# Kernel optimization log

Hardware: AMD Instinct MI355X
Metric: run time of the kernel (lower is better)

## Reference

```python
import jax, jax.numpy as jnp
import numpy as np

N = 50000      # nodes
E = 800000     # edges (before self loops)
F_IN = 128     # num_features
D = 128        # d_graph_layer
L = 3          # n_graph_layer (extra GAT layers after conv1)
DFC = 128      # d_FC_layer
NFC = 2        # n_FC_layer
C = 2          # num_classes
G = 1000       # number of graphs
NEG_SLOPE = 0.2


def setup_inputs() -> dict:
    key = jax.random.key(0)
    ks = jax.random.split(key, 24)
    s = lambda d: 1.0 / np.sqrt(d)
    inp = {
        "x": jax.random.normal(ks[0], (N, F_IN), jnp.float32),
        "energy": jax.random.normal(ks[1], (G, 1), jnp.float32),
        # conv1 params
        "W1": jax.random.normal(ks[2], (F_IN, D), jnp.float32) * s(F_IN),
        "as1": jax.random.normal(ks[3], (D,), jnp.float32) * s(D),
        "ad1": jax.random.normal(ks[4], (D,), jnp.float32) * s(D),
        "b1": jnp.zeros((D,), jnp.float32),
        # stacked convs params
        "Ws": jax.random.normal(ks[5], (L, D, D), jnp.float32) * s(D),
        "ass": jax.random.normal(ks[6], (L, D), jnp.float32) * s(D),
        "ads": jax.random.normal(ks[7], (L, D), jnp.float32) * s(D),
        "bs": jnp.zeros((L, D), jnp.float32),
        # FC head
        "lin0_W": jax.random.normal(ks[8], (D, DFC), jnp.float32) * s(D),
        "lin0_b": jnp.zeros((DFC,), jnp.float32),
        "lin1_W": jax.random.normal(ks[9], (DFC + 1, DFC), jnp.float32) * s(DFC + 1),
        "lin1_b": jnp.zeros((DFC,), jnp.float32),
        "lins_W": jax.random.normal(ks[10], (NFC - 1, DFC, DFC), jnp.float32) * s(DFC),
        "lins_b": jnp.zeros((NFC - 1, DFC), jnp.float32),
        "lin3_W": jax.random.normal(ks[11], (DFC, C), jnp.float32) * s(DFC),
        "lin3_b": jnp.zeros((C,), jnp.float32),
        # graph structure
        "edge_index": jax.random.randint(ks[12], (2, E), 0, N, dtype=jnp.int64),
        "batchs": jnp.sort(jax.random.randint(ks[13], (N,), 0, G, dtype=jnp.int64)),
    }
    return inp


def gat_layer(x, W, a_src, a_dst, b, src, dst):
    # GATConv (heads=1): h = xW; e_ij = LeakyReLU(a_src.h_src + a_dst.h_dst);
    # alpha = softmax over edges grouped by dst; out_i = sum alpha * h_src + b
    h = x @ W                                        # [N, D]
    e = jax.nn.leaky_relu((h @ a_src)[src] + (h @ a_dst)[dst], NEG_SLOPE)  # [E']
    m = jax.ops.segment_max(e, dst, num_segments=N)  # every node has a self loop
    w = jnp.exp(e - m[dst])
    denom = jax.ops.segment_sum(w, dst, num_segments=N)
    alpha = w / denom[dst]
    out = jax.ops.segment_sum(h[src] * alpha[:, None], dst, num_segments=N)
    return out + b


def reference(x, energy, W1, as1, ad1, b1, Ws, ass, ads, bs,
              lin0_W, lin0_b, lin1_W, lin1_b, lins_W, lins_b,
              lin3_W, lin3_b, edge_index, batchs):
    loop = jnp.arange(N, dtype=edge_index.dtype)     # GATConv add_self_loops
    src = jnp.concatenate([edge_index[0], loop])
    dst = jnp.concatenate([edge_index[1], loop])

    h = jax.nn.relu(gat_layer(x, W1, as1, ad1, b1, src, dst))
    for i in range(L):
        h = jax.nn.relu(gat_layer(h, Ws[i], ass[i], ads[i], bs[i], src, dst))

    g = jax.ops.segment_sum(h, batchs, num_segments=G)   # global_add_pool [G, D]
    y = jax.nn.relu(g @ lin0_W + lin0_b)                 # lins[0]
    z = jax.nn.relu(jnp.concatenate([y, energy], axis=1) @ lin1_W + lin1_b)
    z = z + y                                            # residual
    for i in range(NFC - 1):
        z = jax.nn.relu(z @ lins_W[i] + lins_b[i])
    logits = z @ lin3_W + lin3_b
    return jax.nn.log_softmax(logits, axis=1)            # last == 'log'
```

## Files before the change

### kernel.cpp

```cpp
#include <hip/hip_runtime.h>
#include <math.h>

#define NN 50000
#define EE 800000
#define ET 850000
#define DD 128
#define GG 1000
#define SLOPE 0.2f

#define KB   2048
#define NBA  416
#define BSZ  4096
#define NBUK 208

typedef unsigned int  u32;
typedef unsigned short u16;

__device__ __forceinline__ u16 f2h(float f){
  return __builtin_bit_cast(unsigned short, (_Float16)f);
}
__device__ __forceinline__ float hlo(u32 d){
  return (float)__builtin_bit_cast(_Float16, (unsigned short)(d & 0xFFFFu));
}
__device__ __forceinline__ float hhi(u32 d){
  return (float)__builtin_bit_cast(_Float16, (unsigned short)(d >> 16));
}

__global__ void init_k(const int* __restrict__ batchs, int* __restrict__ cnt,
                       int* __restrict__ gstart, int* __restrict__ bcur){
  int n = blockIdx.x*256 + threadIdx.x;
  if (n < NBUK) bcur[n] = 0;
  if (n < NN){
    cnt[n] = 0;
    int b = batchs[n];
    int prev = n ? batchs[n-1] : -1;
    for (int g = prev+1; g <= b; ++g) gstart[g] = n;
    if (n == NN-1){
      for (int g = b+1; g <= GG; ++g) gstart[g] = NN;
    }
  }
}

__global__ void count_k(const int* __restrict__ ei, int* __restrict__ cnt,
                        int* __restrict__ rank){
  int e = blockIdx.x*256 + threadIdx.x;
  if (e < ET){
    int d = (e < EE) ? ei[EE + e] : (e - EE);
    rank[e] = atomicAdd(&cnt[d], 1);
  }
}

__global__ __launch_bounds__(256) void blocksum_k(const int* __restrict__ cnt,
                                                  int* __restrict__ bsum){
  int i = blockIdx.x*256 + threadIdx.x;
  int v = (i < NN) ? cnt[i] : 0;
  #pragma unroll
  for (int o=32;o;o>>=1) v += __shfl_xor(v,o);
  __shared__ int ws[4];
  if ((threadIdx.x & 63) == 0) ws[threadIdx.x>>6] = v;
  __syncthreads();
  if (threadIdx.x == 0) bsum[blockIdx.x] = ws[0]+ws[1]+ws[2]+ws[3];
}

__global__ __launch_bounds__(256) void scanb_k(int* __restrict__ bsum, int nb){
  int tid = threadIdx.x;
  int v = (tid < nb) ? bsum[tid] : 0;
  int lane = tid & 63, wv = tid >> 6;
  int s = v;
  #pragma unroll
  for (int o=1;o<64;o<<=1){ int t = __shfl_up(s,o); if (lane>=o) s += t; }
  __shared__ int ws[4];
  if (lane == 63) ws[wv] = s;
  __syncthreads();
  int woff = 0;
  for (int k=0;k<wv;++k) woff += ws[k];
  if (tid < nb) bsum[tid] = s - v + woff;
}

__global__ __launch_bounds__(256) void scatter_k(const int* __restrict__ cnt,
                                                 const int* __restrict__ bsum,
                                                 int* __restrict__ row_start){
  int i = blockIdx.x*256 + threadIdx.x;
  int v = (i < NN) ? cnt[i] : 0;
  int lane = threadIdx.x & 63, wv = threadIdx.x >> 6;
  int s = v;
  #pragma unroll
  for (int o=1;o<64;o<<=1){ int t = __shfl_up(s,o); if (lane>=o) s += t; }
  __shared__ int ws[4];
  if (lane == 63) ws[wv] = s;
  __syncthreads();
  int woff = 0;
  for (int k=0;k<wv;++k) woff += ws[k];
  int off = s - v + woff + bsum[blockIdx.x];
  if (i < NN) row_start[i] = off;
  if (i == 0) row_start[NN] = ET;
}

__global__ __launch_bounds__(256) void partA_k(const int* __restrict__ ei,
                                               const int* __restrict__ rank,
                                               const int* __restrict__ row_start,
                                               int* __restrict__ bcur,
                                               uint2* __restrict__ stage){
  __shared__ uint2 lpairs[KB];
  __shared__ int lcnt[256], lstart[256], lrun[256], gbase[256];
  __shared__ int ws[4];
  int tid = threadIdx.x;
  int base = blockIdx.x * KB;
  int nE = min(KB, ET - base);
  lcnt[tid] = 0;
  __syncthreads();
  u32 pos_r[KB/256]; u32 src_r[KB/256];
  #pragma unroll
  for (int i=0;i<KB/256;++i){
    int e = base + i*256 + tid;
    u32 p = 0xFFFFFFFFu, s = 0;
    if (e < ET){
      int d, sr;
      if (e < EE){ sr = ei[e]; d = ei[EE + e]; }
      else       { sr = e - EE; d = sr; }
      p = (u32)(row_start[d] + rank[e]);
      s = (u32)sr;
      atomicAdd(&lcnt[p >> 12], 1);
    }
    pos_r[i] = p; src_r[i] = s;
  }
  __syncthreads();
  int v = lcnt[tid];
  int lane = tid & 63, wv = tid >> 6;
  int s = v;
  #pragma unroll
  for (int o=1;o<64;o<<=1){ int t = __shfl_up(s,o); if (lane>=o) s += t; }
  if (lane == 63) ws[wv] = s;
  __syncthreads();
  int woff = 0;
  for (int k=0;k<wv;++k) woff += ws[k];
  int excl = s - v + woff;
  lstart[tid] = excl;
  lrun[tid]   = excl;
  gbase[tid]  = (tid < NBUK && v > 0) ? atomicAdd(&bcur[tid], v) : 0;
  __syncthreads();
  #pragma unroll
  for (int i=0;i<KB/256;++i){
    if (pos_r[i] != 0xFFFFFFFFu){
      int b = pos_r[i] >> 12;
      int slot = atomicAdd(&lrun[b], 1);
      lpairs[slot] = make_uint2(pos_r[i], src_r[i]);
    }
  }
  __syncthreads();
  for (int j = tid; j < nE; j += 256){
    uint2 pr = lpairs[j];
    int b = pr.x >> 12;
    int dest = (b << 12) + gbase[b] + (j - lstart[b]);
    stage[dest] = pr;
  }
}

__global__ __launch_bounds__(256) void partB_k(const uint2* __restrict__ stage,
                                               int* __restrict__ srcs){
  __shared__ int buf[BSZ];
  int b = blockIdx.x, tid = threadIdx.x;
  int base = b << 12;
  int n_b = min(BSZ, ET - base);
  for (int j = tid; j < n_b; j += 256){
    uint2 pr = stage[base + j];
    buf[pr.x - base] = (int)pr.y;
  }
  __syncthreads();
  for (int j = tid; j*4 < n_b; j += 256){
    *(int4*)(srcs + base + j*4) = *(const int4*)(buf + j*4);
  }
}

__global__ __launch_bounds__(256) void gemm128_f_k(const float* __restrict__ A,
                                                   const float* __restrict__ W,
                                                   const float* __restrict__ as,
                                                   const float* __restrict__ ad,
                                                   float* __restrict__ C,
                                                   float* __restrict__ hs,
                                                   float* __restrict__ hd){
  __shared__ float Alt[DD*64];
  __shared__ float Wl[DD*64];
  int tid = threadIdx.x;
  int rbase = blockIdx.x*64;
  for (int it=0; it<8; ++it){
    int i = it*256 + tid;
    int r = i & 63;
    int c4 = i >> 6;
    float4 v = {0.f,0.f,0.f,0.f};
    if (rbase + r < NN) v = *(const float4*)(A + (size_t)(rbase+r)*DD + c4*4);
    Alt[(c4*4+0)*64 + r] = v.x;
    Alt[(c4*4+1)*64 + r] = v.y;
    Alt[(c4*4+2)*64 + r] = v.z;
    Alt[(c4*4+3)*64 + r] = v.w;
  }
  int ry = tid >> 4, cx = tid & 15;
  float hsum[4] = {0.f,0.f,0.f,0.f};
  float hdsum[4] = {0.f,0.f,0.f,0.f};
  for (int jt=0; jt<2; ++jt){
    __syncthreads();
    for (int it=0; it<8; ++it){
      int i = it*256 + tid;
      int k = i >> 4, c4 = i & 15;
      *(float4*)(Wl + k*64 + c4*4) = *(const float4*)(W + k*DD + jt*64 + c4*4);
    }
    __syncthreads();
    float acc[4][4] = {};
    #pragma unroll 8
    for (int k=0;k<DD;++k){
      float4 av = *(const float4*)(Alt + k*64 + ry*4);
      float4 wv = *(const float4*)(Wl + k*64 + cx*4);
      float a[4] = {av.x, av.y, av.z, av.w};
      float b[4] = {wv.x, wv.y, wv.z, wv.w};
      #pragma unroll
      for (int ii=0;ii<4;++ii)
        #pragma unroll
        for (int jj=0;jj<4;++jj)
          acc[ii][jj] += a[ii]*b[jj];
    }
    float4 a_s = *(const float4*)(as + jt*64 + cx*4);
    float4 a_d = *(const float4*)(ad + jt*64 + cx*4);
    #pragma unroll
    for (int ii=0;ii<4;++ii){
      float ds = acc[ii][0]*a_s.x + acc[ii][1]*a_s.y + acc[ii][2]*a_s.z + acc[ii][3]*a_s.w;
      float dd = acc[ii][0]*a_d.x + acc[ii][1]*a_d.y + acc[ii][2]*a_d.z + acc[ii][3]*a_d.w;
      #pragma unroll
      for (int o=1;o<16;o<<=1){ ds += __shfl_xor(ds,o); dd += __shfl_xor(dd,o); }
      hsum[ii] += ds; hdsum[ii] += dd;
    }
    #pragma unroll
    for (int ii=0;ii<4;++ii){
      int r = rbase + ry*4 + ii;
      if (r < NN){
        float4 o = {acc[ii][0], acc[ii][1], acc[ii][2], acc[ii][3]};
        *(float4*)(C + (size_t)r*DD + jt*64 + cx*4) = o;
      }
    }
  }
  if (cx == 0){
    #pragma unroll
    for (int ii=0;ii<4;++ii){
      int r = rbase + ry*4 + ii;
      if (r < NN){ hs[r] = hsum[ii]; hd[r] = hdsum[ii]; }
    }
  }
}

__global__ __launch_bounds__(256) void gemm128_h_k(const float* __restrict__ A,
                                                   const float* __restrict__ W,
                                                   const float* __restrict__ as,
                                                   const float* __restrict__ ad,
                                                   u16* __restrict__ Ch,
                                                   float* __restrict__ hs,
                                                   float* __restrict__ hd){
  __shared__ float Alt[DD*64];
  __shared__ float Wl[DD*64];
  int tid = threadIdx.x;
  int rbase = blockIdx.x*64;
  for (int it=0; it<8; ++it){
    int i = it*256 + tid;
    int r = i & 63;
    int c4 = i >> 6;
    float4 v = {0.f,0.f,0.f,0.f};
    if (rbase + r < NN) v = *(const float4*)(A + (size_t)(rbase+r)*DD + c4*4);
    Alt[(c4*4+0)*64 + r] = v.x;
    Alt[(c4*4+1)*64 + r] = v.y;
    Alt[(c4*4+2)*64 + r] = v.z;
    Alt[(c4*4+3)*64 + r] = v.w;
  }
  int ry = tid >> 4, cx = tid & 15;
  float hsum[4] = {0.f,0.f,0.f,0.f};
  float hdsum[4] = {0.f,0.f,0.f,0.f};
  for (int jt=0; jt<2; ++jt){
    __syncthreads();
    for (int it=0; it<8; ++it){
      int i = it*256 + tid;
      int k = i >> 4, c4 = i & 15;
      *(float4*)(Wl + k*64 + c4*4) = *(const float4*)(W + k*DD + jt*64 + c4*4);
    }
    __syncthreads();
    float acc[4][4] = {};
    #pragma unroll 8
    for (int k=0;k<DD;++k){
      float4 av = *(const float4*)(Alt + k*64 + ry*4);
      float4 wv = *(const float4*)(Wl + k*64 + cx*4);
      float a[4] = {av.x, av.y, av.z, av.w};
      float b[4] = {wv.x, wv.y, wv.z, wv.w};
      #pragma unroll
      for (int ii=0;ii<4;++ii)
        #pragma unroll
        for (int jj=0;jj<4;++jj)
          acc[ii][jj] += a[ii]*b[jj];
    }
    float4 a_s = *(const float4*)(as + jt*64 + cx*4);
    float4 a_d = *(const float4*)(ad + jt*64 + cx*4);
    #pragma unroll
    for (int ii=0;ii<4;++ii){
      float ds = acc[ii][0]*a_s.x + acc[ii][1]*a_s.y + acc[ii][2]*a_s.z + acc[ii][3]*a_s.w;
      float dd = acc[ii][0]*a_d.x + acc[ii][1]*a_d.y + acc[ii][2]*a_d.z + acc[ii][3]*a_d.w;
      #pragma unroll
      for (int o=1;o<16;o<<=1){ ds += __shfl_xor(ds,o); dd += __shfl_xor(dd,o); }
      hsum[ii] += ds; hdsum[ii] += dd;
    }
    #pragma unroll
    for (int ii=0;ii<4;++ii){
      int r = rbase + ry*4 + ii;
      if (r < NN){
        ushort4 o;
        o.x = f2h(acc[ii][0]); o.y = f2h(acc[ii][1]);
        o.z = f2h(acc[ii][2]); o.w = f2h(acc[ii][3]);
        *(ushort4*)(Ch + (size_t)r*DD + jt*64 + cx*4) = o;
      }
    }
  }
  if (cx == 0){
    #pragma unroll
    for (int ii=0;ii<4;++ii){
      int r = rbase + ry*4 + ii;
      if (r < NN){ hs[r] = hsum[ii]; hd[r] = hdsum[ii]; }
    }
  }
}

__global__ __launch_bounds__(256) void gat_agg_f_k(const float* __restrict__ h,
                                                   const float* __restrict__ hs,
                                                   const float* __restrict__ hd,
                                                   const int* __restrict__ row_start,
                                                   const int* __restrict__ srcs,
                                                   const float* __restrict__ bias,
                                                   float* __restrict__ out){
  int node = blockIdx.x*4 + (threadIdx.x >> 6);
  int lane = threadIdx.x & 63;
  if (node >= NN) return;
  int half = lane >> 5;
  int hl   = lane & 31;
  int beg = row_start[node], end = row_start[node+1];
  float hdn = hd[node];
  float m = -INFINITY, denom = 0.f;
  float4 acc = {0.f,0.f,0.f,0.f};
  for (int c=beg; c<end; c+=64){
    int nc = min(64, end-c);
    float e = -INFINITY; int src = 0;
    if (lane < nc){
      src = srcs[c+lane];
      float t = hs[src] + hdn;
      e = (t >= 0.f) ? t : SLOPE*t;
    }
    float cm = e;
    #pragma unroll
    for (int o=32;o;o>>=1) cm = fmaxf(cm, __shfl_xor(cm,o));
    float nm = fmaxf(m, cm);
    float w = (lane < nc) ? expf(e - nm) : 0.f;
    float cs = w;
    #pragma unroll
    for (int o=32;o;o>>=1) cs += __shfl_xor(cs,o);
    float scale = expf(m - nm);
    denom = denom*scale + cs;
    acc.x *= scale; acc.y *= scale; acc.z *= scale; acc.w *= scale;
    m = nm;
    int nh = (nc + 1 - half) >> 1;
    for (int i=0;i<nh;++i){
      int j = 2*i + half;
      float wi = __shfl(w, j);
      int   si = __shfl(src, j);
      float4 hv = *(const float4*)(h + (size_t)si*DD + hl*4);
      acc.x += wi*hv.x; acc.y += wi*hv.y; acc.z += wi*hv.z; acc.w += wi*hv.w;
    }
  }
  acc.x += __shfl_xor(acc.x, 32);
  acc.y += __shfl_xor(acc.y, 32);
  acc.z += __shfl_xor(acc.z, 32);
  acc.w += __shfl_xor(acc.w, 32);
  if (half == 0){
    float inv = 1.f/denom;
    float4 b4 = *(const float4*)(bias + hl*4);
    float4 o4;
    o4.x = fmaxf(acc.x*inv + b4.x, 0.f);
    o4.y = fmaxf(acc.y*inv + b4.y, 0.f);
    o4.z = fmaxf(acc.z*inv + b4.z, 0.f);
    o4.w = fmaxf(acc.w*inv + b4.w, 0.f);
    *(float4*)(out + (size_t)node*DD + hl*4) = o4;
  }
}

__global__ __launch_bounds__(256) void gat_agg_h_k(const u16* __restrict__ hh,
                                                   const float* __restrict__ hs,
                                                   const float* __restrict__ hd,
                                                   const int* __restrict__ row_start,
                                                   const int* __restrict__ srcs,
                                                   const float* __restrict__ bias,
                                                   float* __restrict__ out){
  int node = blockIdx.x*4 + (threadIdx.x >> 6);
  int lane = threadIdx.x & 63;
  if (node >= NN) return;
  int half = lane >> 5;
  int hl   = lane & 31;
  int beg = row_start[node], end = row_start[node+1];
  float hdn = hd[node];
  float m = -INFINITY, denom = 0.f;
  float a0=0.f, a1=0.f, a2=0.f, a3=0.f;
  for (int c=beg; c<end; c+=64){
    int nc = min(64, end-c);
    float e = -INFINITY; int src = 0;
    if (lane < nc){
      src = srcs[c+lane];
      float t = hs[src] + hdn;
      e = (t >= 0.f) ? t : SLOPE*t;
    }
    float cm = e;
    #pragma unroll
    for (int o=32;o;o>>=1) cm = fmaxf(cm, __shfl_xor(cm,o));
    float nm = fmaxf(m, cm);
    float w = (lane < nc) ? expf(e - nm) : 0.f;
    float cs = w;
    #pragma unroll
    for (int o=32;o;o>>=1) cs += __shfl_xor(cs,o);
    float scale = expf(m - nm);
    denom = denom*scale + cs;
    a0 *= scale; a1 *= scale; a2 *= scale; a3 *= scale;
    m = nm;
    int nh = (nc + 1 - half) >> 1;
    for (int i=0;i<nh;++i){
      int j = 2*i + half;
      float wi = __shfl(w, j);
      int   si = __shfl(src, j);
      uint2 hv = *(const uint2*)(hh + (size_t)si*DD + hl*4);
      a0 += wi*hlo(hv.x); a1 += wi*hhi(hv.x);
      a2 += wi*hlo(hv.y); a3 += wi*hhi(hv.y);
    }
  }
  a0 += __shfl_xor(a0, 32);
  a1 += __shfl_xor(a1, 32);
  a2 += __shfl_xor(a2, 32);
  a3 += __shfl_xor(a3, 32);
  if (half == 0){
    float inv = 1.f/denom;
    float4 b4 = *(const float4*)(bias + hl*4);
    float4 o4;
    o4.x = fmaxf(a0*inv + b4.x, 0.f);
    o4.y = fmaxf(a1*inv + b4.y, 0.f);
    o4.z = fmaxf(a2*inv + b4.z, 0.f);
    o4.w = fmaxf(a3*inv + b4.w, 0.f);
    *(float4*)(out + (size_t)node*DD + hl*4) = o4;
  }
}

__global__ __launch_bounds__(128) void tail_k(const float* __restrict__ h,
                                              const int* __restrict__ gstart,
                                              const float* __restrict__ energy,
                                              const float* __restrict__ W0, const float* __restrict__ b0,
                                              const float* __restrict__ W1, const float* __restrict__ b1,
                                              const float* __restrict__ W2, const float* __restrict__ b2,
                                              const float* __restrict__ W3, const float* __restrict__ b3,
                                              float* __restrict__ out){
  __shared__ float row[DD];
  __shared__ float buf[DD];
  int gr = blockIdx.x, j = threadIdx.x;
  int beg = gstart[gr], end = gstart[gr+1];
  float s = 0.f;
  for (int n=beg; n<end; ++n) s += h[(size_t)n*DD + j];
  row[j] = s;
  __syncthreads();
  float acc = 0.f;
  #pragma unroll 8
  for (int k=0;k<DD;++k) acc += row[k]*W0[k*DD + j];
  float y = fmaxf(acc + b0[j], 0.f);
  buf[j] = y;
  __syncthreads();
  acc = 0.f;
  #pragma unroll 8
  for (int k=0;k<DD;++k) acc += buf[k]*W1[k*DD + j];
  acc += energy[gr]*W1[DD*DD + j];
  float z = fmaxf(acc + b1[j], 0.f) + y;
  __syncthreads();
  row[j] = z;
  __syncthreads();
  acc = 0.f;
  #pragma unroll 8
  for (int k=0;k<DD;++k) acc += row[k]*W2[k*DD + j];
  float z2 = fmaxf(acc + b2[j], 0.f);
  buf[j] = z2;
  __syncthreads();
  if (j < 64){
    float z0 = buf[j], z1 = buf[j+64];
    float l0 = z0*W3[j*2]     + z1*W3[(j+64)*2];
    float l1 = z0*W3[j*2 + 1] + z1*W3[(j+64)*2 + 1];
    #pragma unroll
    for (int o=32;o;o>>=1){ l0 += __shfl_xor(l0,o); l1 += __shfl_xor(l1,o); }
    if (j == 0){
      l0 += b3[0]; l1 += b3[1];
      float mx = fmaxf(l0, l1);
      float lse = mx + logf(expf(l0-mx) + expf(l1-mx));
      out[gr*2]   = l0 - lse;
      out[gr*2+1] = l1 - lse;
    }
  }
}

extern "C" void kernel_launch(void* const* d_in, const int* in_sizes, int n_in,
                              void* d_out, int out_size, void* d_ws, size_t ws_size,
                              hipStream_t stream) {
  const float* x      = (const float*)d_in[0];
  const float* energy = (const float*)d_in[1];
  const float* W1     = (const float*)d_in[2];
  const float* as1    = (const float*)d_in[3];
  const float* ad1    = (const float*)d_in[4];
  const float* b1     = (const float*)d_in[5];
  const float* Ws     = (const float*)d_in[6];
  const float* ass    = (const float*)d_in[7];
  const float* ads    = (const float*)d_in[8];
  const float* bs     = (const float*)d_in[9];
  const float* lin0_W = (const float*)d_in[10];
  const float* lin0_b = (const float*)d_in[11];
  const float* lin1_W = (const float*)d_in[12];
  const float* lin1_b = (const float*)d_in[13];
  const float* lins_W = (const float*)d_in[14];
  const float* lins_b = (const float*)d_in[15];
  const float* lin3_W = (const float*)d_in[16];
  const float* lin3_b = (const float*)d_in[17];
  const int*   ei     = (const int*)d_in[18];
  const int*   batchs = (const int*)d_in[19];
  float* out = (float*)d_out;

  char* wp = (char*)d_ws;
  auto alloc = [&](size_t bytes)->void*{
    void* p = (void*)wp;
    wp += (bytes + 255) & ~(size_t)255;
    return p;
  };
  float* hA        = (float*)alloc((size_t)NN*DD*4);
  float* hB        = (float*)alloc((size_t)NN*DD*4);
  u16*   hHf       = (u16*)hB;
  float* hs        = (float*)alloc((size_t)NN*4);
  float* hd        = (float*)alloc((size_t)NN*4);
  int*   cnt       = (int*)alloc((size_t)NN*4);
  int*   row_start = (int*)alloc((size_t)(NN+1)*4);
  int*   rank      = (int*)alloc((size_t)ET*4);
  int*   srcs      = (int*)alloc((size_t)ET*4);
  uint2* stage     = (uint2*)alloc((size_t)NBUK*BSZ*8);
  int*   bcur      = (int*)alloc((size_t)NBUK*4);
  int*   gstart    = (int*)alloc((size_t)(GG+1)*4);
  int*   bsum      = (int*)alloc((size_t)256*4);

  const int NB_N  = (NN + 255)/256;
  const int NB_E  = (ET + 255)/256;
  const int NB_W  = (NN + 3)/4;
  const int NB_G  = (NN + 63)/64;

  init_k<<<NB_N, 256, 0, stream>>>(batchs, cnt, gstart, bcur);
  count_k<<<NB_E, 256, 0, stream>>>(ei, cnt, rank);
  blocksum_k<<<NB_N, 256, 0, stream>>>(cnt, bsum);
  scanb_k<<<1, 256, 0, stream>>>(bsum, NB_N);
  scatter_k<<<NB_N, 256, 0, stream>>>(cnt, bsum, row_start);
  partA_k<<<NBA, 256, 0, stream>>>(ei, rank, row_start, bcur, stage);
  partB_k<<<NBUK, 256, 0, stream>>>(stage, srcs);

  gemm128_f_k<<<NB_G, 256, 0, stream>>>(x, W1, as1, ad1, hB, hs, hd);
  gat_agg_f_k<<<NB_W, 256, 0, stream>>>(hB, hs, hd, row_start, srcs, b1, hA);
  gemm128_f_k<<<NB_G, 256, 0, stream>>>(hA, Ws, ass, ads, hB, hs, hd);
  gat_agg_f_k<<<NB_W, 256, 0, stream>>>(hB, hs, hd, row_start, srcs, bs, hA);

  gemm128_h_k<<<NB_G, 256, 0, stream>>>(hA, Ws + (size_t)1*DD*DD, ass + DD, ads + DD,
                                        hHf, hs, hd);
  gat_agg_h_k<<<NB_W, 256, 0, stream>>>(hHf, hs, hd, row_start, srcs, bs + DD, hA);
  gemm128_h_k<<<NB_G, 256, 0, stream>>>(hA, Ws + (size_t)2*DD*DD, ass + 2*DD, ads + 2*DD,
                                        hHf, hs, hd);
  gat_agg_h_k<<<NB_W, 256, 0, stream>>>(hHf, hs, hd, row_start, srcs, bs + 2*DD, hA);

  tail_k<<<GG, 128, 0, stream>>>(hA, gstart, energy,
                                 lin0_W, lin0_b, lin1_W, lin1_b,
                                 lins_W, lins_b, lin3_W, lin3_b, out);
}
```

Measured before the change: 550.6 us.

## Rewrite node GEMM as register-blocked, double-buffered K-tiled kernel

```diff
diff --git a/kernel.cpp b/kernel.cpp
--- a/kernel.cpp
+++ b/kernel.cpp
@@ -172,152 +172,105 @@
   }
 }
 
-__global__ __launch_bounds__(256) void gemm128_f_k(const float* __restrict__ A,
-                                                   const float* __restrict__ W,
-                                                   const float* __restrict__ as,
-                                                   const float* __restrict__ ad,
-                                                   float* __restrict__ C,
-                                                   float* __restrict__ hs,
-                                                   float* __restrict__ hd){
-  __shared__ float Alt[DD*64];
-  __shared__ float Wl[DD*64];
+template<bool H16>
+__global__ __launch_bounds__(256) void gemm_rb_k(const float* __restrict__ A,
+                                                 const float* __restrict__ W,
+                                                 const float* __restrict__ as,
+                                                 const float* __restrict__ ad,
+                                                 void* __restrict__ Cout,
+                                                 float* __restrict__ hs,
+                                                 float* __restrict__ hd){
+  __shared__ float As[2][16][68];
+  __shared__ float Wsh[2][16][128];
   int tid = threadIdx.x;
   int rbase = blockIdx.x*64;
-  for (int it=0; it<8; ++it){
-    int i = it*256 + tid;
-    int r = i & 63;
-    int c4 = i >> 6;
-    float4 v = {0.f,0.f,0.f,0.f};
-    if (rbase + r < NN) v = *(const float4*)(A + (size_t)(rbase+r)*DD + c4*4);
-    Alt[(c4*4+0)*64 + r] = v.x;
-    Alt[(c4*4+1)*64 + r] = v.y;
-    Alt[(c4*4+2)*64 + r] = v.z;
-    Alt[(c4*4+3)*64 + r] = v.w;
-  }
-  int ry = tid >> 4, cx = tid & 15;
-  float hsum[4] = {0.f,0.f,0.f,0.f};
-  float hdsum[4] = {0.f,0.f,0.f,0.f};
-  for (int jt=0; jt<2; ++jt){
-    __syncthreads();
-    for (int it=0; it<8; ++it){
-      int i = it*256 + tid;
-      int k = i >> 4, c4 = i & 15;
-      *(float4*)(Wl + k*64 + c4*4) = *(const float4*)(W + k*DD + jt*64 + c4*4);
-    }
-    __syncthreads();
-    float acc[4][4] = {};
-    #pragma unroll 8
-    for (int k=0;k<DD;++k){
-      float4 av = *(const float4*)(Alt + k*64 + ry*4);
-      float4 wv = *(const float4*)(Wl + k*64 + cx*4);
-      float a[4] = {av.x, av.y, av.z, av.w};
-      float b[4] = {wv.x, wv.y, wv.z, wv.w};
+  int ty = tid >> 4, tx = tid & 15;
+  int arow = tid >> 2, aq = tid & 3;
+  int wk = tid >> 5, wc = tid & 31;
+
+  float4 aReg, w0Reg, w1Reg;
+  {
+    int r = rbase + arow;
+    aReg = (r < NN) ? *(const float4*)(A + (size_t)r*DD + aq*4) : float4{0,0,0,0};
+    w0Reg = *(const float4*)(W + (size_t)wk*DD + wc*4);
+    w1Reg = *(const float4*)(W + (size_t)(wk+8)*DD + wc*4);
+  }
+  As[0][aq*4+0][arow] = aReg.x;
+  As[0][aq*4+1][arow] = aReg.y;
+  As[0][aq*4+2][arow] = aReg.z;
+  As[0][aq*4+3][arow] = aReg.w;
+  *(float4*)(&Wsh[0][wk][wc*4])   = w0Reg;
+  *(float4*)(&Wsh[0][wk+8][wc*4]) = w1Reg;
+  __syncthreads();
+
+  float acc[4][8] = {};
+  for (int t=0; t<8; ++t){
+    int cur = t & 1;
+    if (t < 7){
+      int k0 = (t+1)*16;
+      int r = rbase + arow;
+      aReg = (r < NN) ? *(const float4*)(A + (size_t)r*DD + k0 + aq*4) : float4{0,0,0,0};
+      w0Reg = *(const float4*)(W + (size_t)(k0+wk)*DD + wc*4);
+      w1Reg = *(const float4*)(W + (size_t)(k0+wk+8)*DD + wc*4);
+    }
+    #pragma unroll
+    for (int k=0;k<16;++k){
+      float4 a4  = *(const float4*)(&As[cur][k][ty*4]);
+      float4 wA  = *(const float4*)(&Wsh[cur][k][tx*8]);
+      float4 wB  = *(const float4*)(&Wsh[cur][k][tx*8+4]);
+      float a[4] = {a4.x, a4.y, a4.z, a4.w};
+      float wv[8] = {wA.x, wA.y, wA.z, wA.w, wB.x, wB.y, wB.z, wB.w};
       #pragma unroll
       for (int ii=0;ii<4;++ii)
         #pragma unroll
-        for (int jj=0;jj<4;++jj)
-          acc[ii][jj] += a[ii]*b[jj];
-    }
-    float4 a_s = *(const float4*)(as + jt*64 + cx*4);
-    float4 a_d = *(const float4*)(ad + jt*64 + cx*4);
-    #pragma unroll
-    for (int ii=0;ii<4;++ii){
-      float ds = acc[ii][0]*a_s.x + acc[ii][1]*a_s.y + acc[ii][2]*a_s.z + acc[ii][3]*a_s.w;
-      float dd = acc[ii][0]*a_d.x + acc[ii][1]*a_d.y + acc[ii][2]*a_d.z + acc[ii][3]*a_d.w;
-      #pragma unroll
-      for (int o=1;o<16;o<<=1){ ds += __shfl_xor(ds,o); dd += __shfl_xor(dd,o); }
-      hsum[ii] += ds; hdsum[ii] += dd;
-    }
-    #pragma unroll
-    for (int ii=0;ii<4;++ii){
-      int r = rbase + ry*4 + ii;
-      if (r < NN){
-        float4 o = {acc[ii][0], acc[ii][1], acc[ii][2], acc[ii][3]};
-        *(float4*)(C + (size_t)r*DD + jt*64 + cx*4) = o;
+        for (int jj=0;jj<8;++jj)
+          acc[ii][jj] += a[ii]*wv[jj];
+    }
+    if (t < 7){
+      __syncthreads();
+      int nxt = cur ^ 1;
+      As[nxt][aq*4+0][arow] = aReg.x;
+      As[nxt][aq*4+1][arow] = aReg.y;
+      As[nxt][aq*4+2][arow] = aReg.z;
+      As[nxt][aq*4+3][arow] = aReg.w;
+      *(float4*)(&Wsh[nxt][wk][wc*4])   = w0Reg;
+      *(float4*)(&Wsh[nxt][wk+8][wc*4]) = w1Reg;
+      __syncthreads();
+    }
+  }
+
+  float4 s0 = *(const float4*)(as + tx*8);
+  float4 s1 = *(const float4*)(as + tx*8 + 4);
+  float4 d0 = *(const float4*)(ad + tx*8);
+  float4 d1 = *(const float4*)(ad + tx*8 + 4);
+  #pragma unroll
+  for (int ii=0;ii<4;++ii){
+    float ds = acc[ii][0]*s0.x + acc[ii][1]*s0.y + acc[ii][2]*s0.z + acc[ii][3]*s0.w
+             + acc[ii][4]*s1.x + acc[ii][5]*s1.y + acc[ii][6]*s1.z + acc[ii][7]*s1.w;
+    float dd = acc[ii][0]*d0.x + acc[ii][1]*d0.y + acc[ii][2]*d0.z + acc[ii][3]*d0.w
+             + acc[ii][4]*d1.x + acc[ii][5]*d1.y + acc[ii][6]*d1.z + acc[ii][7]*d1.w;
+    #pragma unroll
+    for (int o=1;o<16;o<<=1){ ds += __shfl_xor(ds,o); dd += __shfl_xor(dd,o); }
+    int r = rbase + ty*4 + ii;
+    if (tx == 0 && r < NN){ hs[r] = ds; hd[r] = dd; }
+  }
+  #pragma unroll
+  for (int ii=0;ii<4;++ii){
+    int r = rbase + ty*4 + ii;
+    if (r < NN){
+      if constexpr (H16){
+        u16* C = (u16*)Cout;
+        ushort4 o0 = {f2h(acc[ii][0]), f2h(acc[ii][1]), f2h(acc[ii][2]), f2h(acc[ii][3])};
+        ushort4 o1 = {f2h(acc[ii][4]), f2h(acc[ii][5]), f2h(acc[ii][6]), f2h(acc[ii][7])};
+        *(ushort4*)(C + (size_t)r*DD + tx*8)     = o0;
+        *(ushort4*)(C + (size_t)r*DD + tx*8 + 4) = o1;
+      } else {
+        float* C = (float*)Cout;
+        float4 o0 = {acc[ii][0], acc[ii][1], acc[ii][2], acc[ii][3]};
+        float4 o1 = {acc[ii][4], acc[ii][5], acc[ii][6], acc[ii][7]};
+        *(float4*)(C + (size_t)r*DD + tx*8)     = o0;
+        *(float4*)(C + (size_t)r*DD + tx*8 + 4) = o1;
       }
-    }
-  }
-  if (cx == 0){
-    #pragma unroll
-    for (int ii=0;ii<4;++ii){
-      int r = rbase + ry*4 + ii;
-      if (r < NN){ hs[r] = hsum[ii]; hd[r] = hdsum[ii]; }
-    }
-  }
-}
-
-__global__ __launch_bounds__(256) void gemm128_h_k(const float* __restrict__ A,
-                                                   const float* __restrict__ W,
-                                                   const float* __restrict__ as,
-                                                   const float* __restrict__ ad,
-                                                   u16* __restrict__ Ch,
-                                                   float* __restrict__ hs,
-                                                   float* __restrict__ hd){
-  __shared__ float Alt[DD*64];
-  __shared__ float Wl[DD*64];
-  int tid = threadIdx.x;
-  int rbase = blockIdx.x*64;
-  for (int it=0; it<8; ++it){
-    int i = it*256 + tid;
-    int r = i & 63;
-    int c4 = i >> 6;
-    float4 v = {0.f,0.f,0.f,0.f};
-    if (rbase + r < NN) v = *(const float4*)(A + (size_t)(rbase+r)*DD + c4*4);
-    Alt[(c4*4+0)*64 + r] = v.x;
-    Alt[(c4*4+1)*64 + r] = v.y;
-    Alt[(c4*4+2)*64 + r] = v.z;
-    Alt[(c4*4+3)*64 + r] = v.w;
-  }
-  int ry = tid >> 4, cx = tid & 15;
-  float hsum[4] = {0.f,0.f,0.f,0.f};
-  float hdsum[4] = {0.f,0.f,0.f,0.f};
-  for (int jt=0; jt<2; ++jt){
-    __syncthreads();
-    for (int it=0; it<8; ++it){
-      int i = it*256 + tid;
-      int k = i >> 4, c4 = i & 15;
-      *(float4*)(Wl + k*64 + c4*4) = *(const float4*)(W + k*DD + jt*64 + c4*4);
-    }
-    __syncthreads();
-    float acc[4][4] = {};
-    #pragma unroll 8
-    for (int k=0;k<DD;++k){
-      float4 av = *(const float4*)(Alt + k*64 + ry*4);
-      float4 wv = *(const float4*)(Wl + k*64 + cx*4);
-      float a[4] = {av.x, av.y, av.z, av.w};
-      float b[4] = {wv.x, wv.y, wv.z, wv.w};
-      #pragma unroll
-      for (int ii=0;ii<4;++ii)
-        #pragma unroll
-        for (int jj=0;jj<4;++jj)
-          acc[ii][jj] += a[ii]*b[jj];
-    }
-    float4 a_s = *(const float4*)(as + jt*64 + cx*4);
-    float4 a_d = *(const float4*)(ad + jt*64 + cx*4);
-    #pragma unroll
-    for (int ii=0;ii<4;++ii){
-      float ds = acc[ii][0]*a_s.x + acc[ii][1]*a_s.y + acc[ii][2]*a_s.z + acc[ii][3]*a_s.w;
-      float dd = acc[ii][0]*a_d.x + acc[ii][1]*a_d.y + acc[ii][2]*a_d.z + acc[ii][3]*a_d.w;
-      #pragma unroll
-      for (int o=1;o<16;o<<=1){ ds += __shfl_xor(ds,o); dd += __shfl_xor(dd,o); }
-      hsum[ii] += ds; hdsum[ii] += dd;
-    }
-    #pragma unroll
-    for (int ii=0;ii<4;++ii){
-      int r = rbase + ry*4 + ii;
-      if (r < NN){
-        ushort4 o;
-        o.x = f2h(acc[ii][0]); o.y = f2h(acc[ii][1]);
-        o.z = f2h(acc[ii][2]); o.w = f2h(acc[ii][3]);
-        *(ushort4*)(Ch + (size_t)r*DD + jt*64 + cx*4) = o;
-      }
-    }
-  }
-  if (cx == 0){
-    #pragma unroll
-    for (int ii=0;ii<4;++ii){
-      int r = rbase + ry*4 + ii;
-      if (r < NN){ hs[r] = hsum[ii]; hd[r] = hdsum[ii]; }
     }
   }
 }
@@ -555,16 +508,16 @@
   partA_k<<<NBA, 256, 0, stream>>>(ei, rank, row_start, bcur, stage);
   partB_k<<<NBUK, 256, 0, stream>>>(stage, srcs);
 
-  gemm128_f_k<<<NB_G, 256, 0, stream>>>(x, W1, as1, ad1, hB, hs, hd);
+  gemm_rb_k<false><<<NB_G, 256, 0, stream>>>(x, W1, as1, ad1, (void*)hB, hs, hd);
   gat_agg_f_k<<<NB_W, 256, 0, stream>>>(hB, hs, hd, row_start, srcs, b1, hA);
-  gemm128_f_k<<<NB_G, 256, 0, stream>>>(hA, Ws, ass, ads, hB, hs, hd);
+  gemm_rb_k<false><<<NB_G, 256, 0, stream>>>(hA, Ws, ass, ads, (void*)hB, hs, hd);
   gat_agg_f_k<<<NB_W, 256, 0, stream>>>(hB, hs, hd, row_start, srcs, bs, hA);
 
-  gemm128_h_k<<<NB_G, 256, 0, stream>>>(hA, Ws + (size_t)1*DD*DD, ass + DD, ads + DD,
-                                        hHf, hs, hd);
+  gemm_rb_k<true><<<NB_G, 256, 0, stream>>>(hA, Ws + (size_t)1*DD*DD, ass + DD, ads + DD,
+                                            (void*)hHf, hs, hd);
   gat_agg_h_k<<<NB_W, 256, 0, stream>>>(hHf, hs, hd, row_start, srcs, bs + DD, hA);
-  gemm128_h_k<<<NB_G, 256, 0, stream>>>(hA, Ws + (size_t)2*DD*DD, ass + 2*DD, ads + 2*DD,
-                                        hHf, hs, hd);
+  gemm_rb_k<true><<<NB_G, 256, 0, stream>>>(hA, Ws + (size_t)2*DD*DD, ass + 2*DD, ads + 2*DD,
+                                            (void*)hHf, hs, hd);
   gat_agg_h_k<<<NB_W, 256, 0, stream>>>(hHf, hs, hd, row_start, srcs, bs + 2*DD, hA);
 
   tail_k<<<GG, 128, 0, stream>>>(hA, gstart, energy,
```

New measurement: 557.4 us. No clear change (+1.2%).
